# Performance work log

Hardware: AMD Instinct MI355X
Metric: run time of the kernel (lower is better)

Reference implementation:

```python
import jax, jax.numpy as jnp
import numpy as np

NGRID = 32
NTOKEN = NGRID * NGRID          # 1024
HEAD = 4
DK = 64
NLAYER = 4
FDIM = 64
BATCH = 8
DX = 2.0 / (NGRID - 1)          # grid spacing; dx == dy
EPS = 1e-5
SLOPE = 0.01                    # LeakyReLU negative slope (torch default)


def _mlp(e, W0, b0, W1, b1, W2, b2):
    # DenseNet([4,32,64,1], LeakyReLU): act after all but last layer
    h = jax.nn.leaky_relu(e @ W0.T + b0, SLOPE)
    h = jax.nn.leaky_relu(h @ W1.T + b1, SLOPE)
    return (h @ W2.T + b2)[..., 0]  # (n, n)


def _edges():
    xs = jnp.linspace(-1.0, 1.0, NGRID, dtype=jnp.float32)
    grid = jnp.stack(jnp.meshgrid(xs, xs, indexing='ij'), axis=-1).reshape(NTOKEN, 2)
    gi = jnp.broadcast_to(grid[:, None, :], (NTOKEN, NTOKEN, 2))
    gj = jnp.broadcast_to(grid[None, :, :], (NTOKEN, NTOKEN, 2))
    return jnp.concatenate([gi, gj], axis=-1)  # (n, n, 4)


def _ln(x, g, b, axes):
    m = jnp.mean(x, axes, keepdims=True)
    v = jnp.var(x, axes, keepdims=True)
    return (x - m) / jnp.sqrt(v + EPS) * g + b


def _forward(xy, kW0, kb0, kW1, kb1, kW2, kb2,
             fW0, fb0, fW1, fb1, fW2, fb2,
             Wq, bq, Wk, bk, ln0_g, ln0_b, ln_g, ln_b):
    n = NTOKEN
    dxdy = DX * DX
    scale = 1.0 / jnp.sqrt(jnp.float32(DK))
    edge = _edges()
    weight = _mlp(edge, kW0, kb0, kW1, kb1, kW2, kb2)    # (n, n)
    weightf = _mlp(edge, fW0, fb0, fW1, fb1, fW2, fb2)   # (n, n)

    Vin = _ln(xy, ln0_g, ln0_b, (-2, -1))                # LayerNorm over [2n, F]
    for j in range(NLAYER - 1):
        Q = jnp.einsum('bnf,hkf->bhnk', Vin, Wq[j]) + bq[j][None, :, None, :]
        K = jnp.einsum('bnf,hkf->bhnk', Vin, Wk[j]) + bk[j][None, :, None, :]
        A = jnp.einsum('bhnk,bhmk->bhnm', Q, K) * scale  # non-softmax attention
        mid = dxdy * jnp.einsum('bhnm,bmf->bnf', A, Vin) # sum over heads fused
        Vin = _ln(mid, ln_g[j], ln_b[j], (-1,)) + Vin

    j = NLAYER - 1
    Q = jnp.einsum('bnf,hkf->bhnk', Vin, Wq[j]) + bq[j][None, :, None, :]
    K = jnp.einsum('bnf,hkf->bhnk', Vin, Wk[j]) + bk[j][None, :, None, :]
    Kn = K[:, :, :n, :]
    Au = jnp.einsum('bhnk,bhmk->bhnm', Q[:, :, :n, :], Kn) * scale
    Af = jnp.einsum('bhnk,bhmk->bhnm', Q[:, :, n:, :], Kn) * scale
    xu = xy[:, :n, :]
    Vu = dxdy * jnp.einsum('bhnm,bmf->bhfn', Au, xu)     # (B, H, F, n)
    Vf = dxdy * jnp.einsum('bhnm,bmf->bhfn', Af, xu)
    out = dxdy * (jnp.einsum('bhfn,nj->bfj', Vu, weight)
                  + jnp.einsum('bhfn,nj->bfj', Vf, weightf))
    return jnp.transpose(out, (0, 2, 1))                 # (B, out_dim=n, F)


def setup_inputs() -> dict:
    key = jax.random.key(0)
    ks = jax.random.split(key, 24)
    s = 0.05
    d = {
        'xy': jax.random.normal(ks[0], (BATCH, 2 * NTOKEN, FDIM), jnp.float32),
        'kW0': jax.random.normal(ks[1], (32, 4)) * s, 'kb0': jnp.zeros((32,)),
        'kW1': jax.random.normal(ks[2], (64, 32)) * s, 'kb1': jnp.zeros((64,)),
        'kW2': jax.random.normal(ks[3], (1, 64)) * s, 'kb2': jnp.zeros((1,)),
        'fW0': jax.random.normal(ks[4], (32, 4)) * s, 'fb0': jnp.zeros((32,)),
        'fW1': jax.random.normal(ks[5], (64, 32)) * s, 'fb1': jnp.zeros((64,)),
        'fW2': jax.random.normal(ks[6], (1, 64)) * s, 'fb2': jnp.zeros((1,)),
        'Wq': jax.random.normal(ks[7], (NLAYER, HEAD, DK, FDIM)) * s,
        'bq': jax.random.normal(ks[8], (NLAYER, HEAD, DK)) * s,
        'Wk': jax.random.normal(ks[9], (NLAYER, HEAD, DK, FDIM)) * s,
        'bk': jax.random.normal(ks[10], (NLAYER, HEAD, DK)) * s,
        'ln0_g': jnp.ones((2 * NTOKEN, FDIM)), 'ln0_b': jnp.zeros((2 * NTOKEN, FDIM)),
        'ln_g': jnp.ones((NLAYER - 1, FDIM)), 'ln_b': jnp.zeros((NLAYER - 1, FDIM)),
    }
    return d


def reference(xy, kW0, kb0, kW1, kb1, kW2, kb2,
              fW0, fb0, fW1, fb1, fW2, fb2,
              Wq, bq, Wk, bk, ln0_g, ln0_b, ln_g, ln_b):
    return _forward(xy, kW0, kb0, kW1, kb1, kW2, kb2,
                    fW0, fb0, fW1, fb1, fW2, fb2,
                    Wq, bq, Wk, bk, ln0_g, ln0_b, ln_g, ln_b)
```

## Files before the change

kernel.cpp:

```cpp
#include <hip/hip_runtime.h>
#include <math.h>

#define BATCH 8
constexpr float DXC   = 2.0f/31.0f;
constexpr float DXDY  = DXC*DXC;
constexpr float SCALE = 0.125f;
constexpr float EPSC  = 1e-5f;
constexpr float SLOPEC= 0.01f;

#define OFF_LNP    0u
#define OFF_M      256u
#define OFF_U      16640u
#define OFF_V      16896u
#define OFF_C      17152u
#define OFF_WSP2   17168u
#define OFF_VIN    150288u
#define OFF_W      1198864u
#define OFF_WF     2247440u
#define OFF_GPA    3296016u
#define OFF_GSA    4344592u
#define OFF_GPB    4360976u
#define OFF_GSB    5409552u
#define OFF_P      5425936u
#define MP_STRIDE  4352

typedef short bf16x8 __attribute__((ext_vector_type(8)));
typedef float f32x4  __attribute__((ext_vector_type(4)));

struct MlpW {
  const float *kW0,*kb0,*kW1,*kb1,*kW2,*kb2;
  const float *fW0,*fb0,*fW1,*fb1,*fW2,*fb2;
  float *wo, *wfo;
};

__device__ __forceinline__ unsigned cvt2bf(float a, float b){
  unsigned r; asm("v_cvt_pk_bf16_f32 %0, %1, %2" : "=v"(r) : "v"(a), "v"(b)); return r;
}

__device__ __forceinline__ float lrelu(float x){ return fmaxf(x, SLOPEC*x); }

__device__ __forceinline__ float wsum64(float v){
  #pragma unroll
  for(int off=32; off; off>>=1) v += __shfl_xor(v, off);
  return v;
}

__device__ __forceinline__ void mlp_unit(const MlpW P, int unit, int swid, int lane)
{
  int which = unit>>10, i = unit&1023;
  const float* W0 = which? P.fW0:P.kW0; const float* b0 = which? P.fb0:P.kb0;
  const float* W1 = which? P.fW1:P.kW1; const float* b1 = which? P.fb1:P.kb1;
  const float* W2 = which? P.fW2:P.kW2; const float* b2 = which? P.fb2:P.kb2;
  float* outp = which? P.wfo : P.wo;
  int grp = lane>>4, jl = lane&15;
  float xi = -1.f + DXC*(float)(i>>5), yi = -1.f + DXC*(float)(i&31);
  float a0c[8], wxc[8], wyc[8];
  #pragma unroll
  for(int t=0;t<8;t++){
    int c = grp*8+t;
    float4 w0 = *(const float4*)(W0 + c*4);
    a0c[t] = w0.x*xi + w0.y*yi + b0[c];
    wxc[t] = w0.z; wyc[t] = w0.w;
  }
  bf16x8 afr[4];
  #pragma unroll
  for(int ot=0;ot<4;ot++){
    const float* src = W1 + (ot*16+jl)*32 + grp*8;
    uint4 p;
    p.x=cvt2bf(src[0],src[1]); p.y=cvt2bf(src[2],src[3]);
    p.z=cvt2bf(src[4],src[5]); p.w=cvt2bf(src[6],src[7]);
    afr[ot] = __builtin_bit_cast(bf16x8, p);
  }
  float b1v[16], w2v[16];
  #pragma unroll
  for(int ot=0;ot<4;ot++){
    #pragma unroll
    for(int r=0;r<4;r++){
      int o = ot*16 + grp*4 + r;
      b1v[ot*4+r] = b1[o];
      w2v[ot*4+r] = W2[o];
    }
  }
  float b2s = b2[0];
  f32x4 zz = {0.f,0.f,0.f,0.f};
  int jbase = swid*256;
  for(int jt=0;jt<16;jt++){
    int j0 = jbase + jt*16;
    int j  = j0 + jl;
    float xj = -1.f + DXC*(float)(j>>5), yj = -1.f + DXC*(float)(j&31);
    float h[8];
    #pragma unroll
    for(int t=0;t<8;t++){
      float p = a0c[t] + wxc[t]*xj + wyc[t]*yj;
      h[t] = fmaxf(p, SLOPEC*p);
    }
    uint4 hb;
    hb.x=cvt2bf(h[0],h[1]); hb.y=cvt2bf(h[2],h[3]);
    hb.z=cvt2bf(h[4],h[5]); hb.w=cvt2bf(h[6],h[7]);
    bf16x8 bfr = __builtin_bit_cast(bf16x8, hb);
    f32x4 d0 = __builtin_amdgcn_mfma_f32_16x16x32_bf16(afr[0], bfr, zz, 0,0,0);
    f32x4 d1 = __builtin_amdgcn_mfma_f32_16x16x32_bf16(afr[1], bfr, zz, 0,0,0);
    f32x4 d2 = __builtin_amdgcn_mfma_f32_16x16x32_bf16(afr[2], bfr, zz, 0,0,0);
    f32x4 d3 = __builtin_amdgcn_mfma_f32_16x16x32_bf16(afr[3], bfr, zz, 0,0,0);
    float part = 0.f;
    #pragma unroll
    for(int r=0;r<4;r++){
      float s0 = d0[r]+b1v[r];    part = fmaf(w2v[r],    fmaxf(s0,SLOPEC*s0), part);
      float s1 = d1[r]+b1v[4+r];  part = fmaf(w2v[4+r],  fmaxf(s1,SLOPEC*s1), part);
      float s2 = d2[r]+b1v[8+r];  part = fmaf(w2v[8+r],  fmaxf(s2,SLOPEC*s2), part);
      float s3 = d3[r]+b1v[12+r]; part = fmaf(w2v[12+r], fmaxf(s3,SLOPEC*s3), part);
    }
    part += __shfl_xor(part, 16);
    part += __shfl_xor(part, 32);
    if(lane<16) outp[i*1024 + j0 + lane] = part + b2s;
  }
}

__device__ __forceinline__ void transpose_unit(const float* __restrict__ src,
    unsigned short* __restrict__ dst, float* __restrict__ wsp2row,
    int n0, int jj0, unsigned short* S, int utid)
{
  int np = utid&31, jq = utid>>5;
  const float* r0 = src + (size_t)(n0 + 2*np)*1024 + jj0 + jq*8;
  const float* r1 = r0 + 1024;
  float av[8], bv[8];
  *(float4*)&av[0] = *(const float4*)r0;  *(float4*)&av[4] = *(const float4*)(r0+4);
  *(float4*)&bv[0] = *(const float4*)r1;  *(float4*)&bv[4] = *(const float4*)(r1+4);
  unsigned* S32 = (unsigned*)S;
  #pragma unroll
  for(int e=0;e<8;e++)
    S32[((jq*8+e)*72 + 2*np)>>1] = cvt2bf(av[e], bv[e]);
  __syncthreads();
  int jl = utid>>2, seg = utid&3;
  uint4 s0 = *(uint4*)&S[jl*72 + seg*16];
  uint4 s1 = *(uint4*)&S[jl*72 + seg*16 + 8];
  unsigned short* orow = dst + (size_t)(jj0+jl)*1024 + n0 + seg*16;
  *(uint4*)orow = s0;
  *(uint4*)(orow+8) = s1;
  if(utid < 64){
    const unsigned* Sr = (const unsigned*)&S[utid*72];
    float acc = 0.f;
    #pragma unroll
    for(int h=0;h<32;h++){
      unsigned v = Sr[h];
      acc += __builtin_bit_cast(float, v<<16);
      acc += __builtin_bit_cast(float, v & 0xffff0000u);
    }
    wsp2row[jj0 + utid] = acc;
  }
}

__global__ __launch_bounds__(256) void k_pre(
    const float* __restrict__ xy,
    const float* __restrict__ Wq, const float* __restrict__ bq,
    const float* __restrict__ Wk, const float* __restrict__ bk,
    float* __restrict__ ws)
{
  __shared__ float red[8];
  int blk = blockIdx.x, tid = threadIdx.x;
  int lane = tid&63;
  int wid = __builtin_amdgcn_readfirstlane(tid>>6);
  if(blk < 64){
    int j = blk>>4, ch = blk&15;
    float mac[16], uac[16];
    #pragma unroll
    for(int r=0;r<16;r++){ mac[r]=0.f; uac[r]=0.f; }
    float vac=0.f, cac=0.f;
    #pragma unroll 4
    for(int hk=ch*16; hk<ch*16+16; hk++){
      const float* wqrow = Wq + ((size_t)j*256+hk)*64;
      const float* wkrow = Wk + ((size_t)j*256+hk)*64;
      float wkl = wkrow[lane];
      float bkk = bk[j*256+hk], bqk = bq[j*256+hk];
      #pragma unroll
      for(int r=0;r<16;r++){ float wq=wqrow[wid*16+r]; mac[r]+=wq*wkl; uac[r]+=wq*bkk; }
      vac += bqk*wkl; cac += bqk*bkk;
    }
    float* mp = ws + OFF_GPB + (size_t)(j*16+ch)*MP_STRIDE;
    #pragma unroll
    for(int r=0;r<16;r++) mp[(wid*16+r)*64+lane] = mac[r];
    if(lane==0){
      #pragma unroll
      for(int r=0;r<16;r++) mp[4096 + wid*16+r] = uac[r];
    }
    if(wid==0) mp[4160+lane] = vac;
    if(tid==0) mp[4224] = cac;
  } else {
    int bb = blk-64;
    int b = bb>>4, seg = bb&15;
    const float4* x4 = (const float4*)(xy + (size_t)b*131072 + seg*8192);
    float s=0.f, ss=0.f;
    #pragma unroll
    for(int k2=0;k2<8;k2++){
      float4 v = x4[tid + k2*256];
      s  += v.x+v.y+v.z+v.w;
      ss += v.x*v.x+v.y*v.y+v.z*v.z+v.w*v.w;
    }
    s = wsum64(s); ss = wsum64(ss);
    if(lane==0){ red[wid]=s; red[4+wid]=ss; }
    __syncthreads();
    if(tid==0){
      ws[OFF_LNP + (b*16+seg)*2  ] = red[0]+red[1]+red[2]+red[3];
      ws[OFF_LNP + (b*16+seg)*2+1] = red[4]+red[5]+red[6]+red[7];
    }
  }
}

__device__ __forceinline__ void gram_tile8(const float* sA, const float* sB,
    int wid, int lane, float* __restrict__ gp, float* __restrict__ gsp)
{
  float acc[8];
  #pragma unroll
  for(int q=0;q<8;q++) acc[q]=0.f;
  float gsa=0.f;
  for(int m=0;m<64;m++){
    const float4* cp = (const float4*)(sA + m*64 + wid*8);
    float bml = sB[m*64+lane];
    float4 a0=cp[0],a1=cp[1];
    acc[0]+=a0.x*bml; acc[1]+=a0.y*bml; acc[2]+=a0.z*bml; acc[3]+=a0.w*bml;
    acc[4]+=a1.x*bml; acc[5]+=a1.y*bml; acc[6]+=a1.z*bml; acc[7]+=a1.w*bml;
    gsa += bml;
  }
  #pragma unroll
  for(int q=0;q<8;q++) gp[(wid*8+q)*64+lane]=acc[q];
  if(wid==0) gsp[lane]=gsa;
}

__device__ __forceinline__ void build_T8(const float* __restrict__ sG,
    const float* __restrict__ Mj, const float* __restrict__ uj,
    const float* __restrict__ vj, float cj, float gsl,
    int wid, int lane, float* __restrict__ sT, float* __restrict__ stv)
{
  float gv[64];
  #pragma unroll
  for(int c=0;c<64;c++) gv[c]=sG[c*64+lane];
  float tacc = cj*gsl;
  #pragma unroll
  for(int c=0;c<64;c++) tacc += vj[c]*gv[c];
  #pragma unroll
  for(int rr=0;rr<8;rr++){
    int r = wid*8+rr;
    const float* mrow = Mj + r*64;
    float acc = uj[r]*gsl;
    #pragma unroll
    for(int c=0;c<64;c++) acc += mrow[c]*gv[c];
    sT[r*64+lane]=acc;
  }
  if(wid==0) stv[lane]=tacc;
}

__global__ __launch_bounds__(512) void k_ln0ag(const float* __restrict__ xy,
    const float* __restrict__ g, const float* __restrict__ bb,
    const float* __restrict__ lnp,
    float* __restrict__ Vin, float* __restrict__ Gpart, float* __restrict__ gspart,
    MlpW P, int mlp_off, float* __restrict__ ws)
{
  __shared__ float sV[4096];
  int blk = blockIdx.x;
  int tid = threadIdx.x, lane = tid&63;
  int wid = __builtin_amdgcn_readfirstlane(tid>>6);
  if(blk >= 598){
    int j = blk-598;
    const float* mp0 = ws + OFF_GPB + (size_t)(j*16)*MP_STRIDE;
    for(int e=tid; e<1024; e+=512){
      float4 s={0,0,0,0};
      for(int ch=0; ch<16; ch++){
        float4 v = *(const float4*)&mp0[(size_t)ch*MP_STRIDE + e*4];
        s.x+=v.x; s.y+=v.y; s.z+=v.z; s.w+=v.w;
      }
      s.x*=SCALE; s.y*=SCALE; s.z*=SCALE; s.w*=SCALE;
      *(float4*)&ws[OFF_M + j*4096 + e*4] = s;
    }
    if(tid<64){
      float su=0.f, sv=0.f;
      for(int ch=0; ch<16; ch++){
        su += mp0[(size_t)ch*MP_STRIDE + 4096 + tid];
        sv += mp0[(size_t)ch*MP_STRIDE + 4160 + tid];
      }
      ws[OFF_U + j*64+tid] = su*SCALE;
      ws[OFF_V + j*64+tid] = sv*SCALE;
    }
    if(tid==0){
      float sc=0.f;
      for(int ch=0; ch<16; ch++) sc += mp0[(size_t)ch*MP_STRIDE + 4224];
      ws[OFF_C + j] = sc*SCALE;
    }
    return;
  }
  if(blk >= 256){
    mlp_unit(P, mlp_off + (blk-256)*2 + (wid>>2), wid&3, lane);
    return;
  }
  int b = blk>>5, ch = blk&31;
  float s=0.f, ss=0.f;
  #pragma unroll
  for(int k2=0;k2<16;k2++){ s += lnp[(b*16+k2)*2]; ss += lnp[(b*16+k2)*2+1]; }
  float mean = s*(1.0f/131072.0f);
  float var  = ss*(1.0f/131072.0f) - mean*mean;
  float inv  = 1.0f/sqrtf(var+EPSC);
  const float4* x4 = (const float4*)(xy + ((size_t)b*2048 + ch*64)*64);
  const float4* g4 = (const float4*)(g  + (size_t)ch*4096);
  const float4* b4 = (const float4*)(bb + (size_t)ch*4096);
  float4* vo4 = (float4*)(Vin + ((size_t)b*2048 + ch*64)*64);
  float4* sv4 = (float4*)sV;
  #pragma unroll
  for(int e=0;e<2;e++){
    int idx = tid + e*512;
    float4 xv=x4[idx], gv=g4[idx], bv=b4[idx];
    float4 r;
    r.x=(xv.x-mean)*inv*gv.x+bv.x;
    r.y=(xv.y-mean)*inv*gv.y+bv.y;
    r.z=(xv.z-mean)*inv*gv.z+bv.z;
    r.w=(xv.w-mean)*inv*gv.w+bv.w;
    vo4[idx]=r; sv4[idx]=r;
  }
  __syncthreads();
  gram_tile8(sV, sV, wid, lane, Gpart+((size_t)(b*32+ch))*4096, gspart+(b*32+ch)*64);
}

__global__ __launch_bounds__(512) void k_layer(
    float* __restrict__ Vin, const float* __restrict__ xy,
    const float* __restrict__ Gsrc, const float* __restrict__ gssrc,
    float* __restrict__ Gdst, float* __restrict__ gsdst,
    const float* __restrict__ Mg, const float* __restrict__ ug,
    const float* __restrict__ vg, const float* __restrict__ cg,
    const float* __restrict__ lng, const float* __restrict__ lnb,
    int j, int cross, MlpW P, int mlp_off,
    unsigned short* __restrict__ wtg, unsigned short* __restrict__ wftg,
    float* __restrict__ wsp2, int emode)
{
  __shared__ __align__(16) float sV[4096];
  __shared__ __align__(16) float sT[4096];
  __shared__ __align__(16) float sG[4096];
  __shared__ float stv[64];
  int blk = blockIdx.x, tid = threadIdx.x;
  int lane = tid&63;
  int wid = __builtin_amdgcn_readfirstlane(tid>>6);
  if(blk >= 256){
    if(emode == 0){
      mlp_unit(P, mlp_off + (blk-256)*2 + (wid>>2), wid&3, lane);
    } else {
      int half = tid>>8;
      int unit = (blk-256)*2 + half;
      int utid = tid & 255;
      int mat = unit>>8, tile = unit&255;
      int nt = tile>>4, jt = tile&15;
      unsigned short* S = (unsigned short*)(half? sT : sV);
      transpose_unit(mat? P.wfo : P.wo, mat? wftg : wtg,
                     wsp2 + (mat*16 + nt)*1024, nt*64, jt*64, S, utid);
    }
    return;
  }
  int b = blk>>5, ch = blk&31;
  float* vbase = Vin + ((size_t)b*2048 + ch*64)*64;
  {
    const float4* vb4=(const float4*)vbase;
    float4* sv4=(float4*)sV;
    #pragma unroll
    for(int e=0;e<2;e++) sv4[tid+e*512]=vb4[tid+e*512];
  }
  {
    float4 a0={0,0,0,0},a1={0,0,0,0};
    const float4* gp4 = (const float4*)(Gsrc + (size_t)b*32*4096) + tid*2;
    for(int c=0;c<32;c++){
      const float4* p = gp4 + c*1024;
      float4 v0=p[0],v1=p[1];
      a0.x+=v0.x;a0.y+=v0.y;a0.z+=v0.z;a0.w+=v0.w;
      a1.x+=v1.x;a1.y+=v1.y;a1.z+=v1.z;a1.w+=v1.w;
    }
    float4* sg4=(float4*)sG + tid*2;
    sg4[0]=a0; sg4[1]=a1;
  }
  float gsl=0.f;
  for(int c=0;c<32;c++) gsl += gssrc[(b*32+c)*64+lane];
  __syncthreads();
  build_T8(sG, Mg+j*4096, ug+j*64, vg+j*64, cg[j], gsl, wid, lane, sT, stv);
  __syncthreads();
  float Tcol[64];
  #pragma unroll
  for(int c=0;c<64;c++) Tcol[c]=sT[c*64+lane];
  float tvl=stv[lane];
  float gl=lng[j*64+lane], bl=lnb[j*64+lane];
  #pragma unroll
  for(int rr=0;rr<8;rr++){
    int r=wid*8+rr;
    const float4* rp=(const float4*)(sV + r*64);
    float vold = sV[r*64+lane];
    float m=tvl;
    #pragma unroll
    for(int c4=0;c4<16;c4++){
      float4 vv=rp[c4];
      m += vv.x*Tcol[c4*4]+vv.y*Tcol[c4*4+1]+vv.z*Tcol[c4*4+2]+vv.w*Tcol[c4*4+3];
    }
    m*=DXDY;
    float mean=wsum64(m)*(1.f/64.f);
    float d=m-mean;
    float var=wsum64(d*d)*(1.f/64.f);
    float y=d*(1.f/sqrtf(var+EPSC))*gl+bl+vold;
    vbase[r*64+lane]=y;
    sV[r*64+lane]=y;
  }
  __syncthreads();
  if(!cross){
    gram_tile8(sV, sV, wid, lane, Gdst+((size_t)(b*32+ch))*4096, gsdst+(b*32+ch)*64);
  } else if(ch<16){
    const float4* x4=(const float4*)(xy + ((size_t)b*2048+ch*64)*64);
    float4* sx4=(float4*)sG;
    #pragma unroll
    for(int e=0;e<2;e++) sx4[tid+e*512]=x4[tid+e*512];
    __syncthreads();
    gram_tile8(sV, sG, wid, lane, Gdst+((size_t)(b*16+ch))*4096, gsdst+(b*16+ch)*64);
  }
}

__global__ __launch_bounds__(256) void k_pw(
    const unsigned short* __restrict__ WtG, const unsigned short* __restrict__ WftG,
    const float* __restrict__ Vin,
    float* __restrict__ P0, float* __restrict__ P1)
{
  __shared__ __align__(16) unsigned short sVu[64*72];
  __shared__ __align__(16) unsigned short sVf[64*72];
  int bid = blockIdx.x;
  int ns = bid&1, jjc = (bid>>1)&15, b = bid>>5;
  int tid = threadIdx.x, lane = tid&63;
  int wid = __builtin_amdgcn_readfirstlane(tid>>6);
  int jl = lane&15, grp = lane>>4;
  int jjw = jjc*64 + wid*16;
  const float* Vu = Vin + (size_t)b*131072;
  const float* Vf = Vu + 65536;
  f32x4 acc[4] = {{0,0,0,0},{0,0,0,0},{0,0,0,0},{0,0,0,0}};
  int np = tid&31, fq = tid>>5;
  unsigned* Su = (unsigned*)sVu;
  unsigned* Sf = (unsigned*)sVf;
  for(int step=0; step<8; step++){
    int nb = ns*512 + step*64;
    {
      const float* u0 = Vu + (size_t)(nb + 2*np)*64 + fq*8;
      const float* f0 = Vf + (size_t)(nb + 2*np)*64 + fq*8;
      float ua[8], ub[8], fa[8], fb[8];
      *(float4*)&ua[0] = *(const float4*)u0;      *(float4*)&ua[4] = *(const float4*)(u0+4);
      *(float4*)&ub[0] = *(const float4*)(u0+64); *(float4*)&ub[4] = *(const float4*)(u0+68);
      *(float4*)&fa[0] = *(const float4*)f0;      *(float4*)&fa[4] = *(const float4*)(f0+4);
      *(float4*)&fb[0] = *(const float4*)(f0+64); *(float4*)&fb[4] = *(const float4*)(f0+68);
      #pragma unroll
      for(int e=0;e<8;e++){
        Su[((fq*8+e)*72 + 2*np)>>1] = cvt2bf(ua[e], ub[e]);
        Sf[((fq*8+e)*72 + 2*np)>>1] = cvt2bf(fa[e], fb[e]);
      }
    }
    __syncthreads();
    #pragma unroll
    for(int ks=0; ks<2; ks++){
      int kk = ks*32;
      bf16x8 aw  = *(const bf16x8*)&WtG [(size_t)(jjw+jl)*1024 + nb + kk + grp*8];
      bf16x8 awf = *(const bf16x8*)&WftG[(size_t)(jjw+jl)*1024 + nb + kk + grp*8];
      #pragma unroll
      for(int ft=0; ft<4; ft++){
        bf16x8 bu = *(const bf16x8*)&sVu[(ft*16+jl)*72 + kk + grp*8];
        bf16x8 bv = *(const bf16x8*)&sVf[(ft*16+jl)*72 + kk + grp*8];
        acc[ft] = __builtin_amdgcn_mfma_f32_16x16x32_bf16(aw,  bu, acc[ft], 0,0,0);
        acc[ft] = __builtin_amdgcn_mfma_f32_16x16x32_bf16(awf, bv, acc[ft], 0,0,0);
      }
    }
    __syncthreads();
  }
  float* Pd = (ns? P1 : P0) + ((size_t)b*1024 + jjw)*64;
  #pragma unroll
  for(int ft=0; ft<4; ft++){
    #pragma unroll
    for(int r=0;r<4;r++){
      int row = grp*4 + r;
      Pd[(size_t)row*64 + ft*16 + jl] = acc[ft][r];
    }
  }
}

__global__ __launch_bounds__(512) void k_final(
    const float* __restrict__ Gp2, const float* __restrict__ gsp2,
    const float* __restrict__ Mg, const float* __restrict__ ug,
    const float* __restrict__ vg, const float* __restrict__ cg,
    const float* __restrict__ P0, const float* __restrict__ P1,
    const float* __restrict__ wsp2,
    float* __restrict__ out)
{
  __shared__ float sG[4096];
  __shared__ float sT[4096];
  __shared__ float stv[64];
  int blk = blockIdx.x, tid = threadIdx.x;
  int lane = tid&63;
  int wid = __builtin_amdgcn_readfirstlane(tid>>6);
  int b = blk>>5, rg = blk&31;
  {
    float4 a0={0,0,0,0},a1={0,0,0,0};
    const float4* gp4 = (const float4*)(Gp2 + (size_t)b*16*4096) + tid*2;
    for(int c=0;c<16;c++){
      const float4* p = gp4 + c*1024;
      float4 v0=p[0],v1=p[1];
      a0.x+=v0.x;a0.y+=v0.y;a0.z+=v0.z;a0.w+=v0.w;
      a1.x+=v1.x;a1.y+=v1.y;a1.z+=v1.z;a1.w+=v1.w;
    }
    float4* sg4=(float4*)sG + tid*2;
    sg4[0]=a0; sg4[1]=a1;
  }
  float gsl=0.f;
  for(int c=0;c<16;c++) gsl += gsp2[(b*16+c)*64+lane];
  __syncthreads();
  build_T8(sG, Mg+3*4096, ug+3*64, vg+3*64, cg[3], gsl, wid, lane, sT, stv);
  __syncthreads();
  float Tcol[64];
  #pragma unroll
  for(int c=0;c<64;c++) Tcol[c]=sT[c*64+lane];
  float t3l=stv[lane];
  #pragma unroll
  for(int rw=0;rw<4;rw++){
    int jj=rg*32+wid*4+rw;
    float p = P0[((size_t)b*1024+jj)*64+lane]
            + P1[((size_t)b*1024+jj)*64+lane];
    float wsm = 0.f;
    #pragma unroll
    for(int c=0;c<32;c++) wsm += wsp2[c*1024+jj];
    float acc=wsm*t3l;
    #pragma unroll
    for(int c=0;c<64;c++) acc += __shfl(p,c)*Tcol[c];
    out[((size_t)(b*1024)+jj)*64+lane]=acc*(DXDY*DXDY);
  }
}

extern "C" void kernel_launch(void* const* d_in, const int* in_sizes, int n_in,
                              void* d_out, int out_size, void* d_ws, size_t ws_size,
                              hipStream_t stream)
{
  (void)in_sizes; (void)n_in; (void)out_size; (void)ws_size;
  const float* xy   = (const float*)d_in[0];
  const float* kW0  = (const float*)d_in[1];
  const float* kb0  = (const float*)d_in[2];
  const float* kW1  = (const float*)d_in[3];
  const float* kb1  = (const float*)d_in[4];
  const float* kW2  = (const float*)d_in[5];
  const float* kb2  = (const float*)d_in[6];
  const float* fW0  = (const float*)d_in[7];
  const float* fb0  = (const float*)d_in[8];
  const float* fW1  = (const float*)d_in[9];
  const float* fb1  = (const float*)d_in[10];
  const float* fW2  = (const float*)d_in[11];
  const float* fb2  = (const float*)d_in[12];
  const float* Wq   = (const float*)d_in[13];
  const float* bq   = (const float*)d_in[14];
  const float* Wk   = (const float*)d_in[15];
  const float* bk   = (const float*)d_in[16];
  const float* ln0g = (const float*)d_in[17];
  const float* ln0b = (const float*)d_in[18];
  const float* lng  = (const float*)d_in[19];
  const float* lnb  = (const float*)d_in[20];
  float* out = (float*)d_out;
  float* ws  = (float*)d_ws;

  float* lnp    = ws+OFF_LNP;
  float* Mg     = ws+OFF_M;
  float* ug     = ws+OFF_U;
  float* vg     = ws+OFF_V;
  float* cg     = ws+OFF_C;
  float* wsp2   = ws+OFF_WSP2;
  float* Vin    = ws+OFF_VIN;
  float* weight = ws+OFF_W;
  float* weightf= ws+OFF_WF;
  float* GPA    = ws+OFF_GPA;
  float* GSA    = ws+OFF_GSA;
  float* GPB    = ws+OFF_GPB;
  float* GSB    = ws+OFF_GSB;
  unsigned short* Wt  = (unsigned short*)(ws+OFF_P);
  unsigned short* Wft = Wt + 1048576;
  float* P1 = GPB + 524288;

  MlpW P = {kW0,kb0,kW1,kb1,kW2,kb2, fW0,fb0,fW1,fb1,fW2,fb2, weight, weightf};

  k_pre<<<192, 256, 0, stream>>>(xy, Wq, bq, Wk, bk, ws);
  k_ln0ag<<<602, 512, 0, stream>>>(xy, ln0g, ln0b, lnp, Vin, GPA, GSA, P, 0, ws);
  k_layer<<<597, 512, 0, stream>>>(Vin, xy, GPA, GSA, GPB, GSB,
                                   Mg, ug, vg, cg, lng, lnb, 0, 0, P, 684,
                                   Wt, Wft, wsp2, 0);
  k_layer<<<597, 512, 0, stream>>>(Vin, xy, GPB, GSB, GPA, GSA,
                                   Mg, ug, vg, cg, lng, lnb, 1, 0, P, 1366,
                                   Wt, Wft, wsp2, 0);
  k_layer<<<512, 512, 0, stream>>>(Vin, xy, GPA, GSA, GPB, GSB,
                                   Mg, ug, vg, cg, lng, lnb, 2, 1, P, 0,
                                   Wt, Wft, wsp2, 1);

  k_pw<<<256, 256, 0, stream>>>(Wt, Wft, Vin, GPA, P1);
  k_final<<<256, 512, 0, stream>>>(GPB, GSB, Mg, ug, vg, cg, GPA, P1, wsp2, out);
}
```

Measured before the change: 168.1 us.

## Fuse projection GEMM and final output kernel, dropping split-K partials

Merges the bf16 MFMA projection kernel and the final combine kernel into one. Each block now runs the full reduction over tokens and keeps its 64-row result in shared memory, so the partial-product buffers and their global write and read go away. The final T matrix is built per block with 4 waves instead of 8, and the wsp2 column sums are computed once into shared memory. This removes one launch and a round trip through global memory, but halves the grid to 128 blocks and serialises the longer K loop per block, which lowers parallelism.

```diff
diff --git a/kernel.cpp b/kernel.cpp
--- a/kernel.cpp
+++ b/kernel.cpp
@@ -240,6 +240,29 @@
   #pragma unroll
   for(int rr=0;rr<8;rr++){
     int r = wid*8+rr;
+    const float* mrow = Mj + r*64;
+    float acc = uj[r]*gsl;
+    #pragma unroll
+    for(int c=0;c<64;c++) acc += mrow[c]*gv[c];
+    sT[r*64+lane]=acc;
+  }
+  if(wid==0) stv[lane]=tacc;
+}
+
+__device__ __forceinline__ void build_T4(const float* __restrict__ sG,
+    const float* __restrict__ Mj, const float* __restrict__ uj,
+    const float* __restrict__ vj, float cj, float gsl,
+    int wid, int lane, float* __restrict__ sT, float* __restrict__ stv)
+{
+  float gv[64];
+  #pragma unroll
+  for(int c=0;c<64;c++) gv[c]=sG[c*64+lane];
+  float tacc = cj*gsl;
+  #pragma unroll
+  for(int c=0;c<64;c++) tacc += vj[c]*gv[c];
+  #pragma unroll
+  for(int rr=0;rr<16;rr++){
+    int r = wid*16+rr;
     const float* mrow = Mj + r*64;
     float acc = uj[r]*gsl;
     #pragma unroll
@@ -413,27 +436,36 @@
   }
 }
 
-__global__ __launch_bounds__(256) void k_pw(
+__global__ __launch_bounds__(256) void k_pfin(
     const unsigned short* __restrict__ WtG, const unsigned short* __restrict__ WftG,
     const float* __restrict__ Vin,
-    float* __restrict__ P0, float* __restrict__ P1)
-{
-  __shared__ __align__(16) unsigned short sVu[64*72];
-  __shared__ __align__(16) unsigned short sVf[64*72];
+    const float* __restrict__ Gp2, const float* __restrict__ gsp2,
+    const float* __restrict__ Mg, const float* __restrict__ ug,
+    const float* __restrict__ vg, const float* __restrict__ cg,
+    const float* __restrict__ wsp2,
+    float* __restrict__ out)
+{
+  __shared__ __align__(16) unsigned short sStage[2][4608];
+  __shared__ __align__(16) float sG[4096];
+  __shared__ __align__(16) float sT[4096];
+  __shared__ float stv[64];
+  __shared__ float sWsm[64];
   int bid = blockIdx.x;
-  int ns = bid&1, jjc = (bid>>1)&15, b = bid>>5;
+  int jjc = bid&15, b = bid>>4;
   int tid = threadIdx.x, lane = tid&63;
   int wid = __builtin_amdgcn_readfirstlane(tid>>6);
   int jl = lane&15, grp = lane>>4;
   int jjw = jjc*64 + wid*16;
   const float* Vu = Vin + (size_t)b*131072;
   const float* Vf = Vu + 65536;
+  unsigned short* sVu = sStage[0];
+  unsigned short* sVf = sStage[1];
   f32x4 acc[4] = {{0,0,0,0},{0,0,0,0},{0,0,0,0},{0,0,0,0}};
   int np = tid&31, fq = tid>>5;
   unsigned* Su = (unsigned*)sVu;
   unsigned* Sf = (unsigned*)sVf;
-  for(int step=0; step<8; step++){
-    int nb = ns*512 + step*64;
+  for(int step=0; step<16; step++){
+    int nb = step*64;
     {
       const float* u0 = Vu + (size_t)(nb + 2*np)*64 + fq*8;
       const float* f0 = Vf + (size_t)(nb + 2*np)*64 + fq*8;
@@ -464,65 +496,61 @@
     }
     __syncthreads();
   }
-  float* Pd = (ns? P1 : P0) + ((size_t)b*1024 + jjw)*64;
+  float* sD = (float*)sStage;
   #pragma unroll
   for(int ft=0; ft<4; ft++){
     #pragma unroll
     for(int r=0;r<4;r++){
-      int row = grp*4 + r;
-      Pd[(size_t)row*64 + ft*16 + jl] = acc[ft][r];
-    }
-  }
-}
-
-__global__ __launch_bounds__(512) void k_final(
-    const float* __restrict__ Gp2, const float* __restrict__ gsp2,
-    const float* __restrict__ Mg, const float* __restrict__ ug,
-    const float* __restrict__ vg, const float* __restrict__ cg,
-    const float* __restrict__ P0, const float* __restrict__ P1,
-    const float* __restrict__ wsp2,
-    float* __restrict__ out)
-{
-  __shared__ float sG[4096];
-  __shared__ float sT[4096];
-  __shared__ float stv[64];
-  int blk = blockIdx.x, tid = threadIdx.x;
-  int lane = tid&63;
-  int wid = __builtin_amdgcn_readfirstlane(tid>>6);
-  int b = blk>>5, rg = blk&31;
+      int row = wid*16 + grp*4 + r;
+      sD[row*64 + ft*16 + jl] = acc[ft][r];
+    }
+  }
   {
     float4 a0={0,0,0,0},a1={0,0,0,0};
-    const float4* gp4 = (const float4*)(Gp2 + (size_t)b*16*4096) + tid*2;
+    const float4* gp4 = (const float4*)(Gp2 + (size_t)b*16*4096) + tid*4;
     for(int c=0;c<16;c++){
       const float4* p = gp4 + c*1024;
       float4 v0=p[0],v1=p[1];
       a0.x+=v0.x;a0.y+=v0.y;a0.z+=v0.z;a0.w+=v0.w;
       a1.x+=v1.x;a1.y+=v1.y;a1.z+=v1.z;a1.w+=v1.w;
     }
-    float4* sg4=(float4*)sG + tid*2;
+    float4* sg4=(float4*)sG + tid*4;
     sg4[0]=a0; sg4[1]=a1;
+    float4 a2={0,0,0,0},a3={0,0,0,0};
+    for(int c=0;c<16;c++){
+      const float4* p = gp4 + c*1024;
+      float4 v2=p[2],v3=p[3];
+      a2.x+=v2.x;a2.y+=v2.y;a2.z+=v2.z;a2.w+=v2.w;
+      a3.x+=v3.x;a3.y+=v3.y;a3.z+=v3.z;a3.w+=v3.w;
+    }
+    sg4[2]=a2; sg4[3]=a3;
+  }
+  if(tid<64){
+    float s=0.f;
+    #pragma unroll
+    for(int c=0;c<32;c++) s += wsp2[c*1024 + jjc*64 + tid];
+    sWsm[tid]=s;
   }
   float gsl=0.f;
   for(int c=0;c<16;c++) gsl += gsp2[(b*16+c)*64+lane];
   __syncthreads();
-  build_T8(sG, Mg+3*4096, ug+3*64, vg+3*64, cg[3], gsl, wid, lane, sT, stv);
+  build_T4(sG, Mg+3*4096, ug+3*64, vg+3*64, cg[3], gsl, wid, lane, sT, stv);
   __syncthreads();
   float Tcol[64];
   #pragma unroll
   for(int c=0;c<64;c++) Tcol[c]=sT[c*64+lane];
   float t3l=stv[lane];
   #pragma unroll
-  for(int rw=0;rw<4;rw++){
-    int jj=rg*32+wid*4+rw;
-    float p = P0[((size_t)b*1024+jj)*64+lane]
-            + P1[((size_t)b*1024+jj)*64+lane];
-    float wsm = 0.f;
-    #pragma unroll
-    for(int c=0;c<32;c++) wsm += wsp2[c*1024+jj];
-    float acc=wsm*t3l;
-    #pragma unroll
-    for(int c=0;c<64;c++) acc += __shfl(p,c)*Tcol[c];
-    out[((size_t)(b*1024)+jj)*64+lane]=acc*(DXDY*DXDY);
+  for(int t=0;t<16;t++){
+    int jjl = wid*16 + t;
+    const float4* prow = (const float4*)(sD + jjl*64);
+    float accO = sWsm[jjl]*t3l;
+    #pragma unroll
+    for(int c4=0;c4<16;c4++){
+      float4 pv = prow[c4];
+      accO += pv.x*Tcol[c4*4] + pv.y*Tcol[c4*4+1] + pv.z*Tcol[c4*4+2] + pv.w*Tcol[c4*4+3];
+    }
+    out[((size_t)b*1024 + jjc*64 + jjl)*64 + lane] = accO*(DXDY*DXDY);
   }
 }
 
@@ -570,7 +598,6 @@
   float* GSB    = ws+OFF_GSB;
   unsigned short* Wt  = (unsigned short*)(ws+OFF_P);
   unsigned short* Wft = Wt + 1048576;
-  float* P1 = GPB + 524288;
 
   MlpW P = {kW0,kb0,kW1,kb1,kW2,kb2, fW0,fb0,fW1,fb1,fW2,fb2, weight, weightf};
 
@@ -586,6 +613,6 @@
                                    Mg, ug, vg, cg, lng, lnb, 2, 1, P, 0,
                                    Wt, Wft, wsp2, 1);
 
-  k_pw<<<256, 256, 0, stream>>>(Wt, Wft, Vin, GPA, P1);
-  k_final<<<256, 512, 0, stream>>>(GPB, GSB, Mg, ug, vg, cg, GPA, P1, wsp2, out);
-}
+  k_pfin<<<128, 256, 0, stream>>>(Wt, Wft, Vin, GPB, GSB,
+                                  Mg, ug, vg, cg, wsp2, out);
+}
```

After: 188.4 us. 12.1% more time.
